# Performance work log

Measured on AMD Instinct MI355X. Metric: run time of the kernel, lower is better.

The kernel has to match this reference:

```python
import jax, jax.numpy as jnp
import numpy as np

TAU = 1.0 / 30.0
EPS = 1e-12  # matches torch F.normalize clamp_min eps


def _l2norm(x):
    n = jnp.sqrt(jnp.sum(x * x, axis=-1, keepdims=True))
    return x / jnp.maximum(n, EPS)


def setup_inputs() -> dict:
    key = jax.random.key(0)
    ks = jax.random.split(key, 6)
    L, B, D, KD = 4096, 4, 512, 128
    query = jax.random.normal(ks[0], (L, B, D), dtype=jnp.float32)
    k_in = jax.random.normal(ks[1], (L, B, D), dtype=jnp.float32)
    value = jax.random.normal(ks[2], (L, B, D), dtype=jnp.float32)
    # init: normal(0, sqrt(2/out_features)), zero bias
    WK_w = jax.random.normal(ks[3], (KD, D), dtype=jnp.float32) * np.sqrt(2.0 / KD)
    WK_b = jnp.zeros((KD,), dtype=jnp.float32)
    WV_w = jax.random.normal(ks[4], (D, D), dtype=jnp.float32) * np.sqrt(2.0 / D)
    WV_b = jnp.zeros((D,), dtype=jnp.float32)
    return {"query": query, "key": k_in, "value": value,
            "WK_w": WK_w, "WK_b": WK_b, "WV_w": WV_w, "WV_b": WV_b}


def reference(query, key, value, WK_w, WK_b, WV_w, WV_b):
    # query/key/value: [L, B, D]
    wk = _l2norm(key @ WK_w.T + WK_b)      # [Lk, B, KD]
    wq = _l2norm(query @ WK_w.T + WK_b)    # [Lq, B, KD]
    wv = value @ WV_w.T + WV_b             # [Lk, B, D]
    # cosine-similarity scores: [B, Lq, Lk]
    scores = jnp.einsum('qbk,sbk->bqs', wq, wk)
    affinity = jax.nn.softmax(scores / TAU, axis=-1)
    out = jnp.einsum('bqs,sbd->qbd', affinity, wv)  # [Lq, B, D]
    return out
```

## Files before the change

### kernel.cpp

```cpp
#include <hip/hip_runtime.h>

using bf16x8 = __attribute__((ext_vector_type(8))) short;
using u16x8  = __attribute__((ext_vector_type(8))) unsigned short;
using f32x4  = __attribute__((ext_vector_type(4))) float;
using f32x4v = __attribute__((ext_vector_type(4))) float;

__device__ inline unsigned short f2bf(float f) {
  unsigned int u = __builtin_bit_cast(unsigned int, f);
  return (unsigned short)((u + 0x7fffu + ((u >> 16) & 1u)) >> 16);
}

#define MFMA16(a, b, c) __builtin_amdgcn_mfma_f32_16x16x32_bf16((a), (b), (c), 0, 0, 0)

__device__ __forceinline__ void lds_barrier() {
  __builtin_amdgcn_sched_barrier(0);
  asm volatile("s_waitcnt lgkmcnt(0)" ::: "memory");
  __builtin_amdgcn_sched_barrier(0);
  __builtin_amdgcn_s_barrier();
  __builtin_amdgcn_sched_barrier(0);
}

#define LL 4096
#define NB 4
#define DD 512
#define KDIM 128

__global__ __launch_bounds__(256) void proj_qk_kernel(
    const float* __restrict__ Xq, const float* __restrict__ Xk,
    const float* __restrict__ Wk, const float* __restrict__ bk,
    unsigned short* __restrict__ Outq, unsigned short* __restrict__ Outk)
{
  __shared__ char smem[49152];
  char* Xs = smem;
  char* Ws = smem + 16384;

  const int tid = threadIdx.x;
  const int w = tid >> 6, lane = tid & 63, lr = lane & 15, g = lane >> 4;
  const int sel = blockIdx.x & 1;
  const float* X = sel ? Xk : Xq;
  unsigned short* Out = sel ? Outk : Outq;
  const int r0 = (blockIdx.x >> 1) * 64;

  f32x4 acc[8];
  #pragma unroll
  for (int nt = 0; nt < 8; ++nt) acc[nt] = f32x4{0.f, 0.f, 0.f, 0.f};

  for (int kc = 0; kc < 4; ++kc) {
    if (kc) __syncthreads();
    #pragma unroll
    for (int p = 0; p < 4; ++p) {
      int j = tid + p * 256;
      int row = j >> 4, e0 = (j & 15) * 8;
      const float* src = X + (size_t)(r0 + row) * DD + kc * 128 + e0;
      f32x4v f0 = *reinterpret_cast<const f32x4v*>(src);
      f32x4v f1 = *reinterpret_cast<const f32x4v*>(src + 4);
      u16x8 v;
      #pragma unroll
      for (int e = 0; e < 4; ++e) { v[e] = f2bf(f0[e]); v[e + 4] = f2bf(f1[e]); }
      *reinterpret_cast<u16x8*>(Xs + row * 256 + ((e0 * 2) ^ ((row & 7) << 4))) = v;
    }
    #pragma unroll
    for (int p = 0; p < 8; ++p) {
      int j = tid + p * 256;
      int n = j >> 4, e0 = (j & 15) * 8;
      const float* src = Wk + (size_t)n * DD + kc * 128 + e0;
      f32x4v f0 = *reinterpret_cast<const f32x4v*>(src);
      f32x4v f1 = *reinterpret_cast<const f32x4v*>(src + 4);
      u16x8 v;
      #pragma unroll
      for (int e = 0; e < 4; ++e) { v[e] = f2bf(f0[e]); v[e + 4] = f2bf(f1[e]); }
      *reinterpret_cast<u16x8*>(Ws + n * 256 + ((e0 * 2) ^ ((n & 7) << 4))) = v;
    }
    __syncthreads();
    const int arow = w * 16 + lr;
    #pragma unroll
    for (int ks = 0; ks < 4; ++ks) {
      int oa = (ks * 64 + g * 16) ^ ((arow & 7) << 4);
      bf16x8 a = *reinterpret_cast<const bf16x8*>(Xs + arow * 256 + oa);
      #pragma unroll
      for (int nt = 0; nt < 8; ++nt) {
        int n = nt * 16 + lr;
        int ob = (ks * 64 + g * 16) ^ ((n & 7) << 4);
        bf16x8 bb = *reinterpret_cast<const bf16x8*>(Ws + n * 256 + ob);
        acc[nt] = MFMA16(a, bb, acc[nt]);
      }
    }
  }

  float bias[8];
  #pragma unroll
  for (int nt = 0; nt < 8; ++nt) bias[nt] = bk[nt * 16 + lr];
  #pragma unroll
  for (int nt = 0; nt < 8; ++nt)
    #pragma unroll
    for (int i = 0; i < 4; ++i) acc[nt][i] += bias[nt];

  f32x4 ss = f32x4{0.f, 0.f, 0.f, 0.f};
  #pragma unroll
  for (int nt = 0; nt < 8; ++nt)
    #pragma unroll
    for (int i = 0; i < 4; ++i) ss[i] += acc[nt][i] * acc[nt][i];
  #pragma unroll
  for (int m = 1; m < 16; m <<= 1) {
    #pragma unroll
    for (int i = 0; i < 4; ++i) ss[i] += __shfl_xor(ss[i], m);
  }
  float inv[4];
  #pragma unroll
  for (int i = 0; i < 4; ++i) inv[i] = 1.0f / fmaxf(sqrtf(ss[i]), 1e-12f);

  #pragma unroll
  for (int nt = 0; nt < 8; ++nt) {
    int c = nt * 16 + lr;
    #pragma unroll
    for (int i = 0; i < 4; ++i) {
      int r = r0 + w * 16 + g * 4 + i;
      int l = r >> 2, b = r & 3;
      Out[((size_t)(b * LL + l)) * KDIM + c] = f2bf(acc[nt][i] * inv[i]);
    }
  }
}

__global__ __launch_bounds__(256) void proj_v_kernel(
    const float* __restrict__ X, const float* __restrict__ Wv,
    const float* __restrict__ bv, unsigned short* __restrict__ VtOut)
{
  __shared__ char smem[40960];
  char* Xs = smem;
  char* Ws = smem + 32768;

  const int tid = threadIdx.x;
  const int w = tid >> 6, lane = tid & 63, lr = lane & 15, g = lane >> 4;
  const int rb = blockIdx.x >> 3, nb = blockIdx.x & 7;
  const int r0 = rb * 256, d0 = nb * 64;

  f32x4 acc[4][4];
  #pragma unroll
  for (int rt = 0; rt < 4; ++rt)
    #pragma unroll
    for (int nt = 0; nt < 4; ++nt) acc[rt][nt] = f32x4{0.f, 0.f, 0.f, 0.f};

  for (int kc = 0; kc < 8; ++kc) {
    if (kc) __syncthreads();
    #pragma unroll
    for (int p = 0; p < 8; ++p) {
      int j = tid + p * 256;
      int row = j >> 3, e0 = (j & 7) * 8;
      const float* src = X + (size_t)(r0 + row) * DD + kc * 64 + e0;
      f32x4v f0 = *reinterpret_cast<const f32x4v*>(src);
      f32x4v f1 = *reinterpret_cast<const f32x4v*>(src + 4);
      u16x8 v;
      #pragma unroll
      for (int e = 0; e < 4; ++e) { v[e] = f2bf(f0[e]); v[e + 4] = f2bf(f1[e]); }
      *reinterpret_cast<u16x8*>(Xs + row * 128 + ((e0 * 2) ^ ((row & 7) << 4))) = v;
    }
    #pragma unroll
    for (int p = 0; p < 2; ++p) {
      int j = tid + p * 256;
      int n = j >> 3, e0 = (j & 7) * 8;
      const float* src = Wv + (size_t)(d0 + n) * DD + kc * 64 + e0;
      f32x4v f0 = *reinterpret_cast<const f32x4v*>(src);
      f32x4v f1 = *reinterpret_cast<const f32x4v*>(src + 4);
      u16x8 v;
      #pragma unroll
      for (int e = 0; e < 4; ++e) { v[e] = f2bf(f0[e]); v[e + 4] = f2bf(f1[e]); }
      *reinterpret_cast<u16x8*>(Ws + n * 128 + ((e0 * 2) ^ ((n & 7) << 4))) = v;
    }
    __syncthreads();
    #pragma unroll
    for (int ks = 0; ks < 2; ++ks) {
      bf16x8 a[4];
      #pragma unroll
      for (int rt = 0; rt < 4; ++rt) {
        int arow = w * 64 + rt * 16 + lr;
        a[rt] = *reinterpret_cast<const bf16x8*>(
            Xs + arow * 128 + ((ks * 64 + g * 16) ^ ((arow & 7) << 4)));
      }
      #pragma unroll
      for (int nt = 0; nt < 4; ++nt) {
        int n = nt * 16 + lr;
        bf16x8 bb = *reinterpret_cast<const bf16x8*>(
            Ws + n * 128 + ((ks * 64 + g * 16) ^ ((n & 7) << 4)));
        #pragma unroll
        for (int rt = 0; rt < 4; ++rt) acc[rt][nt] = MFMA16(a[rt], bb, acc[rt][nt]);
      }
    }
  }

  __syncthreads();
  float bias[4];
  #pragma unroll
  for (int nt = 0; nt < 4; ++nt) bias[nt] = bv[d0 + nt * 16 + lr];

  unsigned short* Ts = (unsigned short*)smem;
  #pragma unroll
  for (int rt = 0; rt < 4; ++rt)
    #pragma unroll
    for (int nt = 0; nt < 4; ++nt) {
      int dl = nt * 16 + lr;
      #pragma unroll
      for (int i = 0; i < 4; ++i) {
        int rl = w * 64 + rt * 16 + g * 4 + i;
        Ts[dl * 256 + (rl ^ ((dl & 31) << 1))] = f2bf(acc[rt][nt][i] + bias[nt]);
      }
    }
  __syncthreads();

  int bsel = tid >> 6, dl = tid & 63;
  int l0 = r0 >> 2;
  #pragma unroll
  for (int jj = 0; jj < 8; ++jj) {
    u16x8 v;
    #pragma unroll
    for (int e = 0; e < 8; ++e) {
      int rl = (jj * 8 + e) * 4 + bsel;
      v[e] = Ts[dl * 256 + (rl ^ ((dl & 31) << 1))];
    }
    *reinterpret_cast<u16x8*>(VtOut + ((size_t)(bsel * DD + d0 + dl)) * LL + l0 + jj * 8) = v;
  }
}

#define QBLK 64
#define KBLK 64
#define NIT (LL / KBLK)

template<bool DOPV, bool TAIL>
__device__ __forceinline__ void attn_body(
    int tS, const unsigned short* __restrict__ Kp,
    const unsigned short* __restrict__ Vp,
    const char* kcur, char* knxt, const char* prd, char* pwr,
    const bf16x8 (&qf)[4], bf16x8 (&vst)[4][2],
    u16x8 (&kstW)[2], u16x8 (&kstL)[2],
    f32x4 (&acc)[4][4], float (&lsum)[4],
    int lr, int g, int w, int wq, int ws, int r0k, int c0k)
{
  const int tK2 = TAIL ? tS : tS + 2;
  const int tV1 = TAIL ? tS : tS + 1;

  {
    const unsigned short* src = Kp + ((size_t)(tK2 * KBLK + r0k)) * KDIM + c0k;
    kstL[0] = *reinterpret_cast<const u16x8*>(src);
    kstL[1] = *reinterpret_cast<const u16x8*>(src + 32 * KDIM);
  }

  bf16x8 kb[2][4];
  #pragma unroll
  for (int sch = 0; sch < 2; ++sch) {
    int sr = ws * 32 + sch * 16 + lr;
    #pragma unroll
    for (int kc = 0; kc < 4; ++kc)
      kb[sch][kc] = *reinterpret_cast<const bf16x8*>(
          kcur + sr * 256 + ((kc * 64 + g * 16) ^ ((sr & 7) << 4)));
  }
  bf16x8 pf[2][2];
  if (DOPV) {
    #pragma unroll
    for (int qt = 0; qt < 2; ++qt) {
      int q = qt * 16 + lr, swz = (q & 7) << 4;
      pf[qt][0] = *reinterpret_cast<const bf16x8*>(prd + q * 128 + ((g * 16) ^ swz));
      pf[qt][1] = *reinterpret_cast<const bf16x8*>(prd + q * 128 + ((64 + g * 16) ^ swz));
    }
  }
  __builtin_amdgcn_sched_barrier(0);
  asm volatile("s_waitcnt lgkmcnt(0)" ::: "memory");
  __builtin_amdgcn_sched_barrier(0);

  f32x4 s0 = f32x4{0.f, 0.f, 0.f, 0.f};
  f32x4 s1 = f32x4{0.f, 0.f, 0.f, 0.f};
  __builtin_amdgcn_s_setprio(1);
  #pragma unroll
  for (int kc = 0; kc < 4; ++kc) {
    s0 = MFMA16(qf[kc], kb[0][kc], s0);
    s1 = MFMA16(qf[kc], kb[1][kc], s1);
  }
  if (DOPV) {
    #pragma unroll
    for (int qt = 0; qt < 2; ++qt)
      #pragma unroll
      for (int ch = 0; ch < 4; ++ch) {
        acc[qt][ch] = MFMA16(pf[qt][0], vst[ch][0], acc[qt][ch]);
        acc[qt][ch] = MFMA16(pf[qt][1], vst[ch][1], acc[qt][ch]);
      }
  }
  __builtin_amdgcn_s_setprio(0);

  if (DOPV) {
    bf16x8 pf2[2][2];
    #pragma unroll
    for (int qt = 0; qt < 2; ++qt) {
      int q = (qt + 2) * 16 + lr, swz = (q & 7) << 4;
      pf2[qt][0] = *reinterpret_cast<const bf16x8*>(prd + q * 128 + ((g * 16) ^ swz));
      pf2[qt][1] = *reinterpret_cast<const bf16x8*>(prd + q * 128 + ((64 + g * 16) ^ swz));
    }
    __builtin_amdgcn_sched_barrier(0);
    asm volatile("s_waitcnt lgkmcnt(0)" ::: "memory");
    __builtin_amdgcn_sched_barrier(0);
    __builtin_amdgcn_s_setprio(1);
    #pragma unroll
    for (int qt = 0; qt < 2; ++qt)
      #pragma unroll
      for (int ch = 0; ch < 4; ++ch) {
        acc[qt + 2][ch] = MFMA16(pf2[qt][0], vst[ch][0], acc[qt + 2][ch]);
        acc[qt + 2][ch] = MFMA16(pf2[qt][1], vst[ch][1], acc[qt + 2][ch]);
      }
    __builtin_amdgcn_s_setprio(0);
  }

  #pragma unroll
  for (int ch = 0; ch < 4; ++ch)
    #pragma unroll
    for (int sc = 0; sc < 2; ++sc)
      vst[ch][sc] = *reinterpret_cast<const bf16x8*>(
          Vp + (size_t)(w * 64 + ch * 16 + lr) * LL + tV1 * KBLK + sc * 32 + g * 8);

  const int sr0 = ws * 32 + lr, sr1 = sr0 + 16;
  #pragma unroll
  for (int i = 0; i < 4; ++i) {
    float p0 = exp2f(fmaf(s0[i], 43.280851f, -44.723546f));
    float p1 = exp2f(fmaf(s1[i], 43.280851f, -44.723546f));
    lsum[i] += p0 + p1;
    int q = wq * 16 + g * 4 + i, swz = (q & 7) << 4;
    *(unsigned short*)(pwr + q * 128 + ((sr0 * 2) ^ swz)) = f2bf(p0);
    *(unsigned short*)(pwr + q * 128 + ((sr1 * 2) ^ swz)) = f2bf(p1);
  }

  {
    int swz = (r0k & 7) << 4;
    *reinterpret_cast<u16x8*>(knxt + r0k * 256 + ((c0k * 2) ^ swz)) = kstW[0];
    *reinterpret_cast<u16x8*>(knxt + (r0k + 32) * 256 + ((c0k * 2) ^ swz)) = kstW[1];
  }
  lds_barrier();
}

__global__ __launch_bounds__(512, 2) void attn_kernel(
    const unsigned short* __restrict__ Qn, const unsigned short* __restrict__ Kn,
    const unsigned short* __restrict__ Vt, float* __restrict__ Out)
{
  __shared__ char smem[49664];
  char* Ks0 = smem;
  char* Ks1 = smem + 16384;
  char* Ps0 = smem + 32768;
  char* Ps1 = smem + 40960;
  float* Ls = (float*)(smem + 49152);

  const int tid = threadIdx.x;
  const int w = tid >> 6, lane = tid & 63, lr = lane & 15, g = lane >> 4;
  const int wq = w & 3, ws = w >> 2;
  const int r0k = tid >> 4, c0k = (tid & 15) * 8;

  const int bid = blockIdx.x;
  const int b = (bid & 7) >> 1;
  const int tile = ((bid >> 3) << 1) | (bid & 1);
  const int q0 = tile * QBLK;

  const unsigned short* Kp = Kn + (size_t)b * LL * KDIM;
  const unsigned short* Vp = Vt + (size_t)b * DD * LL;

  bf16x8 qf[4];
  {
    const unsigned short* qp = Qn + ((size_t)(b * LL + q0 + wq * 16 + lr)) * KDIM + g * 8;
    #pragma unroll
    for (int kc = 0; kc < 4; ++kc)
      qf[kc] = *reinterpret_cast<const bf16x8*>(qp + kc * 32);
  }

  f32x4 acc[4][4];
  #pragma unroll
  for (int qt = 0; qt < 4; ++qt)
    #pragma unroll
    for (int ch = 0; ch < 4; ++ch) acc[qt][ch] = f32x4{0.f, 0.f, 0.f, 0.f};
  float lsum[4] = {0.f, 0.f, 0.f, 0.f};

  bf16x8 vstA[4][2], vstB[4][2];
  u16x8 kstE[2], kstO[2];

  {
    u16x8 k0 = *reinterpret_cast<const u16x8*>(Kp + (size_t)r0k * KDIM + c0k);
    u16x8 k1 = *reinterpret_cast<const u16x8*>(Kp + (size_t)(r0k + 32) * KDIM + c0k);
    int swz = (r0k & 7) << 4;
    *reinterpret_cast<u16x8*>(Ks0 + r0k * 256 + ((c0k * 2) ^ swz)) = k0;
    *reinterpret_cast<u16x8*>(Ks0 + (r0k + 32) * 256 + ((c0k * 2) ^ swz)) = k1;
    #pragma unroll
    for (int ch = 0; ch < 4; ++ch)
      #pragma unroll
      for (int sc = 0; sc < 2; ++sc)
        vstA[ch][sc] = *reinterpret_cast<const bf16x8*>(
            Vp + (size_t)(w * 64 + ch * 16 + lr) * LL + sc * 32 + g * 8);
    const unsigned short* src = Kp + ((size_t)(1 * KBLK + r0k)) * KDIM + c0k;
    kstO[0] = *reinterpret_cast<const u16x8*>(src);
    kstO[1] = *reinterpret_cast<const u16x8*>(src + 32 * KDIM);
  }
  __syncthreads();

  attn_body<false, false>(0, Kp, Vp, Ks0, Ks1, Ps1, Ps0, qf, vstB, kstO, kstE,
                          acc, lsum, lr, g, w, wq, ws, r0k, c0k);

  for (int t = 1; t < 63; t += 2) {
    attn_body<true, false>(t,     Kp, Vp, Ks1, Ks0, Ps0, Ps1, qf, vstA, kstE, kstO,
                           acc, lsum, lr, g, w, wq, ws, r0k, c0k);
    attn_body<true, false>(t + 1, Kp, Vp, Ks0, Ks1, Ps1, Ps0, qf, vstB, kstO, kstE,
                           acc, lsum, lr, g, w, wq, ws, r0k, c0k);
  }
  attn_body<true, true>(63, Kp, Vp, Ks1, Ks0, Ps0, Ps1, qf, vstA, kstE, kstO,
                        acc, lsum, lr, g, w, wq, ws, r0k, c0k);

  #pragma unroll
  for (int qt = 0; qt < 4; ++qt) {
    int q = qt * 16 + lr, swz = (q & 7) << 4;
    bf16x8 pa0 = *reinterpret_cast<const bf16x8*>(Ps1 + q * 128 + ((g * 16) ^ swz));
    bf16x8 pa1 = *reinterpret_cast<const bf16x8*>(Ps1 + q * 128 + ((64 + g * 16) ^ swz));
    #pragma unroll
    for (int ch = 0; ch < 4; ++ch) {
      acc[qt][ch] = MFMA16(pa0, vstB[ch][0], acc[qt][ch]);
      acc[qt][ch] = MFMA16(pa1, vstB[ch][1], acc[qt][ch]);
    }
  }

  #pragma unroll
  for (int m = 1; m < 16; m <<= 1) {
    #pragma unroll
    for (int i = 0; i < 4; ++i) lsum[i] += __shfl_xor(lsum[i], m);
  }
  if (lr == 0) {
    #pragma unroll
    for (int i = 0; i < 4; ++i) Ls[ws * 64 + wq * 16 + g * 4 + i] = lsum[i];
  }
  __syncthreads();

  #pragma unroll
  for (int qt = 0; qt < 4; ++qt) {
    float linv[4];
    #pragma unroll
    for (int i = 0; i < 4; ++i) {
      int q = qt * 16 + g * 4 + i;
      linv[i] = 1.0f / (Ls[q] + Ls[64 + q]);
    }
    #pragma unroll
    for (int ch = 0; ch < 4; ++ch) {
      int d = w * 64 + ch * 16 + lr;
      #pragma unroll
      for (int i = 0; i < 4; ++i) {
        int q = q0 + qt * 16 + g * 4 + i;
        Out[((size_t)q * NB + b) * DD + d] = acc[qt][ch][i] * linv[i];
      }
    }
  }
}

extern "C" void kernel_launch(void* const* d_in, const int* in_sizes, int n_in,
                              void* d_out, int out_size, void* d_ws, size_t ws_size,
                              hipStream_t stream) {
  const float* query = (const float*)d_in[0];
  const float* key   = (const float*)d_in[1];
  const float* value = (const float*)d_in[2];
  const float* WKw   = (const float*)d_in[3];
  const float* WKb   = (const float*)d_in[4];
  const float* WVw   = (const float*)d_in[5];
  const float* WVb   = (const float*)d_in[6];
  float* out = (float*)d_out;

  unsigned short* wqn = (unsigned short*)d_ws;
  unsigned short* wkn = wqn + (size_t)NB * LL * KDIM;
  unsigned short* vt  = wkn + (size_t)NB * LL * KDIM;

  proj_qk_kernel<<<512, 256, 0, stream>>>(query, key, WKw, WKb, wqn, wkn);
  proj_v_kernel <<<512, 256, 0, stream>>>(value, WVw, WVb, vt);
  attn_kernel   <<<256, 512, 0, stream>>>(wqn, wkn, vt, out);
}
```

Measured before the change: 213.8 us.

## Load K fragments straight from global into registers, drop LDS K staging

Instead of staging each K tile through double-buffered LDS with a swizzled store and reload, each wave now loads its K MFMA fragments directly from global memory into registers one step ahead. V prefetch depth drops from two register buffers to one, and the PV MFMAs for all four query tiles are merged into a single phase after one LDS wait. This cuts LDS traffic and shared memory size, which could allow more occupancy, but it issues redundant, less coalesced global loads of K (both query-wave groups read the same rows) and shortens the latency hiding for V loads.

```diff
diff --git a/kernel.cpp b/kernel.cpp
--- a/kernel.cpp
+++ b/kernel.cpp
@@ -224,46 +224,27 @@
 #define KBLK 64
 #define NIT (LL / KBLK)
 
-template<bool DOPV, bool TAIL>
-__device__ __forceinline__ void attn_body(
-    int tS, const unsigned short* __restrict__ Kp,
+template<bool DOPV>
+__device__ __forceinline__ void attn_step10(
+    int t, const unsigned short* __restrict__ Kp,
     const unsigned short* __restrict__ Vp,
-    const char* kcur, char* knxt, const char* prd, char* pwr,
-    const bf16x8 (&qf)[4], bf16x8 (&vst)[4][2],
-    u16x8 (&kstW)[2], u16x8 (&kstL)[2],
+    const char* prd, char* pwr,
+    const bf16x8 (&qf)[4], bf16x8 (&kb)[2][4], bf16x8 (&vst)[4][2],
     f32x4 (&acc)[4][4], float (&lsum)[4],
-    int lr, int g, int w, int wq, int ws, int r0k, int c0k)
+    int lr, int g, int w, int wq, int ws)
 {
-  const int tK2 = TAIL ? tS : tS + 2;
-  const int tV1 = TAIL ? tS : tS + 1;
-
-  {
-    const unsigned short* src = Kp + ((size_t)(tK2 * KBLK + r0k)) * KDIM + c0k;
-    kstL[0] = *reinterpret_cast<const u16x8*>(src);
-    kstL[1] = *reinterpret_cast<const u16x8*>(src + 32 * KDIM);
-  }
-
-  bf16x8 kb[2][4];
-  #pragma unroll
-  for (int sch = 0; sch < 2; ++sch) {
-    int sr = ws * 32 + sch * 16 + lr;
-    #pragma unroll
-    for (int kc = 0; kc < 4; ++kc)
-      kb[sch][kc] = *reinterpret_cast<const bf16x8*>(
-          kcur + sr * 256 + ((kc * 64 + g * 16) ^ ((sr & 7) << 4)));
-  }
-  bf16x8 pf[2][2];
+  bf16x8 pf[4][2];
   if (DOPV) {
     #pragma unroll
-    for (int qt = 0; qt < 2; ++qt) {
-      int q = qt * 16 + lr, swz = (q & 7) << 4;
-      pf[qt][0] = *reinterpret_cast<const bf16x8*>(prd + q * 128 + ((g * 16) ^ swz));
-      pf[qt][1] = *reinterpret_cast<const bf16x8*>(prd + q * 128 + ((64 + g * 16) ^ swz));
-    }
-  }
-  __builtin_amdgcn_sched_barrier(0);
-  asm volatile("s_waitcnt lgkmcnt(0)" ::: "memory");
-  __builtin_amdgcn_sched_barrier(0);
+    for (int qt = 0; qt < 4; ++qt) {
+      int q = qt * 16 + lr, sw = (q & 7) << 4;
+      pf[qt][0] = *reinterpret_cast<const bf16x8*>(prd + q * 128 + ((g * 16) ^ sw));
+      pf[qt][1] = *reinterpret_cast<const bf16x8*>(prd + q * 128 + ((64 + g * 16) ^ sw));
+    }
+    __builtin_amdgcn_sched_barrier(0);
+    asm volatile("s_waitcnt lgkmcnt(0)" ::: "memory");
+    __builtin_amdgcn_sched_barrier(0);
+  }
 
   f32x4 s0 = f32x4{0.f, 0.f, 0.f, 0.f};
   f32x4 s1 = f32x4{0.f, 0.f, 0.f, 0.f};
@@ -275,7 +256,7 @@
   }
   if (DOPV) {
     #pragma unroll
-    for (int qt = 0; qt < 2; ++qt)
+    for (int qt = 0; qt < 4; ++qt)
       #pragma unroll
       for (int ch = 0; ch < 4; ++ch) {
         acc[qt][ch] = MFMA16(pf[qt][0], vst[ch][0], acc[qt][ch]);
@@ -284,34 +265,21 @@
   }
   __builtin_amdgcn_s_setprio(0);
 
-  if (DOPV) {
-    bf16x8 pf2[2][2];
-    #pragma unroll
-    for (int qt = 0; qt < 2; ++qt) {
-      int q = (qt + 2) * 16 + lr, swz = (q & 7) << 4;
-      pf2[qt][0] = *reinterpret_cast<const bf16x8*>(prd + q * 128 + ((g * 16) ^ swz));
-      pf2[qt][1] = *reinterpret_cast<const bf16x8*>(prd + q * 128 + ((64 + g * 16) ^ swz));
-    }
-    __builtin_amdgcn_sched_barrier(0);
-    asm volatile("s_waitcnt lgkmcnt(0)" ::: "memory");
-    __builtin_amdgcn_sched_barrier(0);
-    __builtin_amdgcn_s_setprio(1);
-    #pragma unroll
-    for (int qt = 0; qt < 2; ++qt)
-      #pragma unroll
-      for (int ch = 0; ch < 4; ++ch) {
-        acc[qt + 2][ch] = MFMA16(pf2[qt][0], vst[ch][0], acc[qt + 2][ch]);
-        acc[qt + 2][ch] = MFMA16(pf2[qt][1], vst[ch][1], acc[qt + 2][ch]);
-      }
-    __builtin_amdgcn_s_setprio(0);
-  }
-
+  const int tn = (t + 1 < NIT) ? t + 1 : NIT - 1;
+  #pragma unroll
+  for (int sch = 0; sch < 2; ++sch) {
+    int sr = ws * 32 + sch * 16 + lr;
+    #pragma unroll
+    for (int kc = 0; kc < 4; ++kc)
+      kb[sch][kc] = *reinterpret_cast<const bf16x8*>(
+          Kp + ((size_t)(tn * KBLK + sr)) * KDIM + kc * 32 + g * 8);
+  }
   #pragma unroll
   for (int ch = 0; ch < 4; ++ch)
     #pragma unroll
     for (int sc = 0; sc < 2; ++sc)
       vst[ch][sc] = *reinterpret_cast<const bf16x8*>(
-          Vp + (size_t)(w * 64 + ch * 16 + lr) * LL + tV1 * KBLK + sc * 32 + g * 8);
+          Vp + (size_t)(w * 64 + ch * 16 + lr) * LL + t * KBLK + sc * 32 + g * 8);
 
   const int sr0 = ws * 32 + lr, sr1 = sr0 + 16;
   #pragma unroll
@@ -319,16 +287,11 @@
     float p0 = exp2f(fmaf(s0[i], 43.280851f, -44.723546f));
     float p1 = exp2f(fmaf(s1[i], 43.280851f, -44.723546f));
     lsum[i] += p0 + p1;
-    int q = wq * 16 + g * 4 + i, swz = (q & 7) << 4;
-    *(unsigned short*)(pwr + q * 128 + ((sr0 * 2) ^ swz)) = f2bf(p0);
-    *(unsigned short*)(pwr + q * 128 + ((sr1 * 2) ^ swz)) = f2bf(p1);
-  }
-
-  {
-    int swz = (r0k & 7) << 4;
-    *reinterpret_cast<u16x8*>(knxt + r0k * 256 + ((c0k * 2) ^ swz)) = kstW[0];
-    *reinterpret_cast<u16x8*>(knxt + (r0k + 32) * 256 + ((c0k * 2) ^ swz)) = kstW[1];
-  }
+    int q = wq * 16 + g * 4 + i, sw = (q & 7) << 4;
+    *(unsigned short*)(pwr + q * 128 + ((sr0 * 2) ^ sw)) = f2bf(p0);
+    *(unsigned short*)(pwr + q * 128 + ((sr1 * 2) ^ sw)) = f2bf(p1);
+  }
+
   lds_barrier();
 }
 
@@ -336,17 +299,14 @@
     const unsigned short* __restrict__ Qn, const unsigned short* __restrict__ Kn,
     const unsigned short* __restrict__ Vt, float* __restrict__ Out)
 {
-  __shared__ char smem[49664];
-  char* Ks0 = smem;
-  char* Ks1 = smem + 16384;
-  char* Ps0 = smem + 32768;
-  char* Ps1 = smem + 40960;
-  float* Ls = (float*)(smem + 49152);
+  __shared__ char smem[16896];
+  char* Ps0 = smem;
+  char* Ps1 = smem + 8192;
+  float* Ls = (float*)(smem + 16384);
 
   const int tid = threadIdx.x;
   const int w = tid >> 6, lane = tid & 63, lr = lane & 15, g = lane >> 4;
   const int wq = w & 3, ws = w >> 2;
-  const int r0k = tid >> 4, c0k = (tid & 15) * 8;
 
   const int bid = blockIdx.x;
   const int b = (bid & 7) >> 1;
@@ -371,48 +331,36 @@
     for (int ch = 0; ch < 4; ++ch) acc[qt][ch] = f32x4{0.f, 0.f, 0.f, 0.f};
   float lsum[4] = {0.f, 0.f, 0.f, 0.f};
 
-  bf16x8 vstA[4][2], vstB[4][2];
-  u16x8 kstE[2], kstO[2];
-
-  {
-    u16x8 k0 = *reinterpret_cast<const u16x8*>(Kp + (size_t)r0k * KDIM + c0k);
-    u16x8 k1 = *reinterpret_cast<const u16x8*>(Kp + (size_t)(r0k + 32) * KDIM + c0k);
-    int swz = (r0k & 7) << 4;
-    *reinterpret_cast<u16x8*>(Ks0 + r0k * 256 + ((c0k * 2) ^ swz)) = k0;
-    *reinterpret_cast<u16x8*>(Ks0 + (r0k + 32) * 256 + ((c0k * 2) ^ swz)) = k1;
-    #pragma unroll
-    for (int ch = 0; ch < 4; ++ch)
-      #pragma unroll
-      for (int sc = 0; sc < 2; ++sc)
-        vstA[ch][sc] = *reinterpret_cast<const bf16x8*>(
-            Vp + (size_t)(w * 64 + ch * 16 + lr) * LL + sc * 32 + g * 8);
-    const unsigned short* src = Kp + ((size_t)(1 * KBLK + r0k)) * KDIM + c0k;
-    kstO[0] = *reinterpret_cast<const u16x8*>(src);
-    kstO[1] = *reinterpret_cast<const u16x8*>(src + 32 * KDIM);
+  bf16x8 kb[2][4];
+  bf16x8 vst[4][2];
+
+  #pragma unroll
+  for (int sch = 0; sch < 2; ++sch) {
+    int sr = ws * 32 + sch * 16 + lr;
+    #pragma unroll
+    for (int kc = 0; kc < 4; ++kc)
+      kb[sch][kc] = *reinterpret_cast<const bf16x8*>(
+          Kp + (size_t)sr * KDIM + kc * 32 + g * 8);
   }
   __syncthreads();
 
-  attn_body<false, false>(0, Kp, Vp, Ks0, Ks1, Ps1, Ps0, qf, vstB, kstO, kstE,
-                          acc, lsum, lr, g, w, wq, ws, r0k, c0k);
+  attn_step10<false>(0, Kp, Vp, Ps1, Ps0, qf, kb, vst, acc, lsum, lr, g, w, wq, ws);
 
   for (int t = 1; t < 63; t += 2) {
-    attn_body<true, false>(t,     Kp, Vp, Ks1, Ks0, Ps0, Ps1, qf, vstA, kstE, kstO,
-                           acc, lsum, lr, g, w, wq, ws, r0k, c0k);
-    attn_body<true, false>(t + 1, Kp, Vp, Ks0, Ks1, Ps1, Ps0, qf, vstB, kstO, kstE,
-                           acc, lsum, lr, g, w, wq, ws, r0k, c0k);
-  }
-  attn_body<true, true>(63, Kp, Vp, Ks1, Ks0, Ps0, Ps1, qf, vstA, kstE, kstO,
-                        acc, lsum, lr, g, w, wq, ws, r0k, c0k);
+    attn_step10<true>(t,     Kp, Vp, Ps0, Ps1, qf, kb, vst, acc, lsum, lr, g, w, wq, ws);
+    attn_step10<true>(t + 1, Kp, Vp, Ps1, Ps0, qf, kb, vst, acc, lsum, lr, g, w, wq, ws);
+  }
+  attn_step10<true>(63, Kp, Vp, Ps0, Ps1, qf, kb, vst, acc, lsum, lr, g, w, wq, ws);
 
   #pragma unroll
   for (int qt = 0; qt < 4; ++qt) {
-    int q = qt * 16 + lr, swz = (q & 7) << 4;
-    bf16x8 pa0 = *reinterpret_cast<const bf16x8*>(Ps1 + q * 128 + ((g * 16) ^ swz));
-    bf16x8 pa1 = *reinterpret_cast<const bf16x8*>(Ps1 + q * 128 + ((64 + g * 16) ^ swz));
+    int q = qt * 16 + lr, sw = (q & 7) << 4;
+    bf16x8 pa0 = *reinterpret_cast<const bf16x8*>(Ps1 + q * 128 + ((g * 16) ^ sw));
+    bf16x8 pa1 = *reinterpret_cast<const bf16x8*>(Ps1 + q * 128 + ((64 + g * 16) ^ sw));
     #pragma unroll
     for (int ch = 0; ch < 4; ++ch) {
-      acc[qt][ch] = MFMA16(pa0, vstB[ch][0], acc[qt][ch]);
-      acc[qt][ch] = MFMA16(pa1, vstB[ch][1], acc[qt][ch]);
+      acc[qt][ch] = MFMA16(pa0, vst[ch][0], acc[qt][ch]);
+      acc[qt][ch] = MFMA16(pa1, vst[ch][1], acc[qt][ch]);
     }
   }
 
```

After: 313.2 us. +46.4%, slower.
